# Performance work log

Hardware: AMD Instinct MI355X
Metric: run time of the kernel (lower is better)

Reference implementation:

```python
import jax, jax.numpy as jnp
import numpy as np

B, N, T, C = 2, 2048, 32, 32
NUM_BASES, MAX_K, K_CURR = 4, 32, 16


def setup_inputs() -> dict:
    key = jax.random.key(0)
    k1, k2, k3, k4, k5 = jax.random.split(key, 5)
    z = jax.random.normal(k1, (B, N, T, C), dtype=jnp.float32)
    neighbor_indices = jax.random.randint(k2, (N, K_CURR), 0, N)
    # parameters (match torch init scales)
    adjacency = 0.5 + 0.01 * jax.random.normal(k3, (N, MAX_K), dtype=jnp.float32)
    basis_weights = 0.02 * jax.random.normal(k4, (NUM_BASES, N, MAX_K), dtype=jnp.float32)
    channel_coeffs = jax.random.normal(k5, (C, NUM_BASES), dtype=jnp.float32)
    return {
        "z": z,
        "neighbor_indices": neighbor_indices,
        "adjacency": adjacency,
        "basis_weights": basis_weights,
        "channel_coeffs": channel_coeffs,
    }


def reference(z, neighbor_indices, adjacency, basis_weights, channel_coeffs):
    # z: [B,N,T,C], neighbor_indices: [N,k]
    k = neighbor_indices.shape[1]
    bases = basis_weights[:, :, :k]        # [num_bases, N, k]
    adj = adjacency[:, :k]                 # [N, k]
    # per-channel effective edge weights: [C, N, k]
    eff = jnp.einsum('cb,bnk->cnk', channel_coeffs, bases)
    edge_w = eff * adj[None, :, :]         # [C, N, k]
    w = jnp.transpose(edge_w, (1, 2, 0))   # [N, k, C]
    # gather neighbor features: [B, N, k, T, C]
    z_neigh = z[:, neighbor_indices]
    # weighted sum over neighbors, per-channel weights
    out = jnp.einsum('bnktc,nkc->bntc', z_neigh, w)
    return jnp.tanh(out)
```

## Files before the change

kernel.cpp:

```cpp
#include <hip/hip_runtime.h>


constexpr int BB_    = 2;
constexpr int NN_    = 2048;
constexpr int TT_    = 32;
constexpr int CC_    = 32;
constexpr int NBASE_ = 4;
constexpr int MAXK_  = 32;
constexpr int KC_    = 16;

__device__ __forceinline__ float fast_tanh(float x) {
    float e = __expf(2.0f * x);
    float r = __builtin_amdgcn_rcpf(e + 1.0f);
    return fmaf(-2.0f, r, 1.0f);
}

__global__ __launch_bounds__(256) void cgl_kernel(
    const float* __restrict__ z,
    const int*   __restrict__ nbr,
    const float* __restrict__ adj,
    const float* __restrict__ bw,
    const float* __restrict__ cc,
    float*       __restrict__ out)
{
    __shared__ __align__(16) float w_s[KC_][CC_];
    __shared__ float bw_s[NBASE_][KC_];
    __shared__ float cc_s[CC_ * NBASE_];
    __shared__ float adj_s[KC_];
    __shared__ int   idx_s[KC_];

    const int tid = threadIdx.x;
    const int blk = blockIdx.x;
    const int b   = blk >> 11;
    const int n   = blk & (NN_ - 1);

    if (tid < NBASE_ * KC_) {
        int bb = tid >> 4, k = tid & 15;
        bw_s[bb][k] = bw[((size_t)bb * NN_ + n) * MAXK_ + k];
    } else if (tid >= 64 && tid < 64 + CC_ * NBASE_) {
        int i = tid - 64;
        cc_s[i] = cc[i];
    } else if (tid >= 192 && tid < 192 + KC_) {
        int k = tid - 192;
        adj_s[k] = adj[(size_t)n * MAXK_ + k];
        idx_s[k] = nbr[n * KC_ + k];
    }
    __syncthreads();

    {
        int i = tid;
        #pragma unroll
        for (int r = 0; r < 2; ++r, i += 256) {
            int k = i >> 5, c = i & 31;
            float s = cc_s[c * NBASE_ + 0] * bw_s[0][k]
                    + cc_s[c * NBASE_ + 1] * bw_s[1][k]
                    + cc_s[c * NBASE_ + 2] * bw_s[2][k]
                    + cc_s[c * NBASE_ + 3] * bw_s[3][k];
            w_s[k][c] = s * adj_s[k];
        }
    }
    __syncthreads();

    const int c0 = (tid << 2) & 31;
    const float4* __restrict__ z4 = (const float4*)z;
    const size_t zb = (size_t)b * NN_ * (TT_ * CC_ / 4);

    float4 acc = make_float4(0.f, 0.f, 0.f, 0.f);
    #pragma unroll
    for (int k = 0; k < KC_; ++k) {
        const int nk = idx_s[k];
        float4 zv = z4[zb + (size_t)nk * (TT_ * CC_ / 4) + tid];
        float4 wv = *(const float4*)&w_s[k][c0];
        acc.x = fmaf(zv.x, wv.x, acc.x);
        acc.y = fmaf(zv.y, wv.y, acc.y);
        acc.z = fmaf(zv.z, wv.z, acc.z);
        acc.w = fmaf(zv.w, wv.w, acc.w);
    }

    float4 o;
    o.x = fast_tanh(acc.x);
    o.y = fast_tanh(acc.y);
    o.z = fast_tanh(acc.z);
    o.w = fast_tanh(acc.w);
    ((float4*)out)[(size_t)blk * 256 + tid] = o;
}

extern "C" void kernel_launch(void* const* d_in, const int* in_sizes, int n_in,
                              void* d_out, int out_size, void* d_ws, size_t ws_size,
                              hipStream_t stream) {
    const float* z   = (const float*)d_in[0];
    const int*   nbr = (const int*)d_in[1];
    const float* adj = (const float*)d_in[2];
    const float* bw  = (const float*)d_in[3];
    const float* cc  = (const float*)d_in[4];
    float* out = (float*)d_out;

    cgl_kernel<<<dim3(BB_ * NN_), dim3(256), 0, stream>>>(z, nbr, adj, bw, cc, out);
}
```

Measured before the change: 96.64 us.

## Remap blocks so each XCD owns one batch and time-quarter slice of z

Each block now handles four nodes (one per wave) for one batch and one quarter of the time axis. The batch and time-quarter are taken from the low three bits of the block index, so under round-robin dispatch each of the eight XCDs touches only its own slice of z. The intent is to make the random neighbor gathers hit in each XCD's private L2 instead of spreading the whole z tensor over every cache. The per-node edge weight setup is now done four times per block and each time slice is recomputed across blocks, which adds redundant setup work and relies on an assumed dispatch order.

```diff
diff --git a/kernel.cpp b/kernel.cpp
--- a/kernel.cpp
+++ b/kernel.cpp
@@ -8,6 +8,10 @@
 constexpr int NBASE_ = 4;
 constexpr int MAXK_  = 32;
 constexpr int KC_    = 16;
+
+constexpr int TQ_      = 4;
+constexpr int SLICE_F4 = (TT_ / TQ_) * CC_ / 4;
+constexpr int NODES_PB = 4;
 
 __device__ __forceinline__ float fast_tanh(float x) {
     float e = __expf(2.0f * x);
@@ -23,54 +27,67 @@
     const float* __restrict__ cc,
     float*       __restrict__ out)
 {
-    __shared__ __align__(16) float w_s[KC_][CC_];
-    __shared__ float bw_s[NBASE_][KC_];
-    __shared__ float cc_s[CC_ * NBASE_];
-    __shared__ float adj_s[KC_];
-    __shared__ int   idx_s[KC_];
+    __shared__ __align__(16) float w_s[NODES_PB][KC_][CC_];
+    __shared__ float bw_s[NODES_PB][NBASE_][KC_];
+    __shared__ float cc_s[NBASE_ * CC_];
+    __shared__ float adj_s[NODES_PB][KC_];
+    __shared__ int   idx_s[NODES_PB][KC_];
 
     const int tid = threadIdx.x;
     const int blk = blockIdx.x;
-    const int b   = blk >> 11;
-    const int n   = blk & (NN_ - 1);
 
-    if (tid < NBASE_ * KC_) {
-        int bb = tid >> 4, k = tid & 15;
-        bw_s[bb][k] = bw[((size_t)bb * NN_ + n) * MAXK_ + k];
-    } else if (tid >= 64 && tid < 64 + CC_ * NBASE_) {
-        int i = tid - 64;
-        cc_s[i] = cc[i];
-    } else if (tid >= 192 && tid < 192 + KC_) {
-        int k = tid - 192;
-        adj_s[k] = adj[(size_t)n * MAXK_ + k];
-        idx_s[k] = nbr[n * KC_ + k];
+    const int xcd   = blk & 7;
+    const int b     = xcd >> 2;
+    const int tq    = xcd & 3;
+    const int group = blk >> 3;
+    const int node0 = group * NODES_PB;
+
+    {
+        int nd = tid >> 6, bb = (tid >> 4) & 3, k = tid & 15;
+        bw_s[nd][bb][k] = bw[((size_t)bb * NN_ + (node0 + nd)) * MAXK_ + k];
+
+        if (tid < 64) {
+            int nd2 = tid >> 4, k2 = tid & 15;
+            adj_s[nd2][k2] = adj[(size_t)(node0 + nd2) * MAXK_ + k2];
+        } else if (tid < 128) {
+            int i = tid - 64, nd2 = i >> 4, k2 = i & 15;
+            idx_s[nd2][k2] = nbr[(node0 + nd2) * KC_ + k2];
+        } else {
+            int i = tid - 128, bb2 = i >> 5, c2 = i & 31;
+            cc_s[bb2 * CC_ + c2] = cc[c2 * NBASE_ + bb2];
+        }
     }
     __syncthreads();
 
     {
         int i = tid;
         #pragma unroll
-        for (int r = 0; r < 2; ++r, i += 256) {
-            int k = i >> 5, c = i & 31;
-            float s = cc_s[c * NBASE_ + 0] * bw_s[0][k]
-                    + cc_s[c * NBASE_ + 1] * bw_s[1][k]
-                    + cc_s[c * NBASE_ + 2] * bw_s[2][k]
-                    + cc_s[c * NBASE_ + 3] * bw_s[3][k];
-            w_s[k][c] = s * adj_s[k];
+        for (int r = 0; r < 8; ++r, i += 256) {
+            int nd = i >> 9, k = (i >> 5) & 15, c = i & 31;
+            float s = cc_s[0 * CC_ + c] * bw_s[nd][0][k]
+                    + cc_s[1 * CC_ + c] * bw_s[nd][1][k]
+                    + cc_s[2 * CC_ + c] * bw_s[nd][2][k]
+                    + cc_s[3 * CC_ + c] * bw_s[nd][3][k];
+            w_s[nd][k][c] = s * adj_s[nd][k];
         }
     }
     __syncthreads();
 
-    const int c0 = (tid << 2) & 31;
+    const int wave = tid >> 6;
+    const int lane = tid & 63;
+    const int n    = node0 + wave;
+    const int c0   = (lane << 2) & 31;
+
     const float4* __restrict__ z4 = (const float4*)z;
-    const size_t zb = (size_t)b * NN_ * (TT_ * CC_ / 4);
+    const size_t plane = (size_t)(TT_ * CC_ / 4);
+    const size_t zb    = (size_t)b * NN_ * plane + (size_t)tq * SLICE_F4 + lane;
 
     float4 acc = make_float4(0.f, 0.f, 0.f, 0.f);
     #pragma unroll
     for (int k = 0; k < KC_; ++k) {
-        const int nk = idx_s[k];
-        float4 zv = z4[zb + (size_t)nk * (TT_ * CC_ / 4) + tid];
-        float4 wv = *(const float4*)&w_s[k][c0];
+        const int nk = idx_s[wave][k];
+        float4 zv = z4[zb + (size_t)nk * plane];
+        float4 wv = *(const float4*)&w_s[wave][k][c0];
         acc.x = fmaf(zv.x, wv.x, acc.x);
         acc.y = fmaf(zv.y, wv.y, acc.y);
         acc.z = fmaf(zv.z, wv.z, acc.z);
@@ -82,7 +99,8 @@
     o.y = fast_tanh(acc.y);
     o.z = fast_tanh(acc.z);
     o.w = fast_tanh(acc.w);
-    ((float4*)out)[(size_t)blk * 256 + tid] = o;
+
+    ((float4*)out)[(size_t)b * NN_ * plane + (size_t)n * plane + tq * SLICE_F4 + lane] = o;
 }
 
 extern "C" void kernel_launch(void* const* d_in, const int* in_sizes, int n_in,
@@ -95,5 +113,6 @@
     const float* cc  = (const float*)d_in[4];
     float* out = (float*)d_out;
 
-    cgl_kernel<<<dim3(BB_ * NN_), dim3(256), 0, stream>>>(z, nbr, adj, bw, cc, out);
+    cgl_kernel<<<dim3(BB_ * TQ_ * (NN_ / NODES_PB)), dim3(256), 0, stream>>>(
+        z, nbr, adj, bw, cc, out);
 }
```

Result: faster. 89.49 us (-7.4%).

## Issue neighbor gathers before weight sync using scalar-loaded indices

Applied to the files above, without the earlier changes.

Each thread now reads the neighbor indices straight from global memory into scalar registers via readfirstlane, so it no longer waits on a shared-memory index table. It issues all 16 gathered z loads before the barrier, overlapping them with the edge-weight computation. The channel-coefficient shared array is transposed for conflict-free reads, and launch bounds ask for 4 blocks per CU. The cost is 64 extra VGPRs for the buffered loads, which may reduce occupancy.

```diff
diff --git a/kernel.cpp b/kernel.cpp
--- a/kernel.cpp
+++ b/kernel.cpp
@@ -15,7 +15,7 @@
     return fmaf(-2.0f, r, 1.0f);
 }
 
-__global__ __launch_bounds__(256) void cgl_kernel(
+__global__ __launch_bounds__(256, 4) void cgl_kernel(
     const float* __restrict__ z,
     const int*   __restrict__ nbr,
     const float* __restrict__ adj,
@@ -25,9 +25,8 @@
 {
     __shared__ __align__(16) float w_s[KC_][CC_];
     __shared__ float bw_s[NBASE_][KC_];
-    __shared__ float cc_s[CC_ * NBASE_];
+    __shared__ float cc_s[NBASE_][CC_];
     __shared__ float adj_s[KC_];
-    __shared__ int   idx_s[KC_];
 
     const int tid = threadIdx.x;
     const int blk = blockIdx.x;
@@ -37,14 +36,20 @@
     if (tid < NBASE_ * KC_) {
         int bb = tid >> 4, k = tid & 15;
         bw_s[bb][k] = bw[((size_t)bb * NN_ + n) * MAXK_ + k];
-    } else if (tid >= 64 && tid < 64 + CC_ * NBASE_) {
-        int i = tid - 64;
-        cc_s[i] = cc[i];
+    } else if (tid < 64 + NBASE_ * CC_) {
+        int i = tid - 64, bb = i >> 5, c = i & 31;
+        cc_s[bb][c] = cc[c * NBASE_ + bb];
     } else if (tid >= 192 && tid < 192 + KC_) {
         int k = tid - 192;
         adj_s[k] = adj[(size_t)n * MAXK_ + k];
-        idx_s[k] = nbr[n * KC_ + k];
     }
+
+    const int* __restrict__ ip = nbr + n * KC_;
+    int nks[KC_];
+    #pragma unroll
+    for (int k = 0; k < KC_; ++k)
+        nks[k] = __builtin_amdgcn_readfirstlane(ip[k]);
+
     __syncthreads();
 
     {
@@ -52,29 +57,32 @@
         #pragma unroll
         for (int r = 0; r < 2; ++r, i += 256) {
             int k = i >> 5, c = i & 31;
-            float s = cc_s[c * NBASE_ + 0] * bw_s[0][k]
-                    + cc_s[c * NBASE_ + 1] * bw_s[1][k]
-                    + cc_s[c * NBASE_ + 2] * bw_s[2][k]
-                    + cc_s[c * NBASE_ + 3] * bw_s[3][k];
+            float s = cc_s[0][c] * bw_s[0][k]
+                    + cc_s[1][c] * bw_s[1][k]
+                    + cc_s[2][c] * bw_s[2][k]
+                    + cc_s[3][c] * bw_s[3][k];
             w_s[k][c] = s * adj_s[k];
         }
     }
+
+    const float4* __restrict__ z4 =
+        (const float4*)z + (size_t)b * NN_ * (TT_ * CC_ / 4);
+    float4 zv[KC_];
+    #pragma unroll
+    for (int k = 0; k < KC_; ++k)
+        zv[k] = z4[(size_t)nks[k] * (TT_ * CC_ / 4) + tid];
+
     __syncthreads();
 
     const int c0 = (tid << 2) & 31;
-    const float4* __restrict__ z4 = (const float4*)z;
-    const size_t zb = (size_t)b * NN_ * (TT_ * CC_ / 4);
-
     float4 acc = make_float4(0.f, 0.f, 0.f, 0.f);
     #pragma unroll
     for (int k = 0; k < KC_; ++k) {
-        const int nk = idx_s[k];
-        float4 zv = z4[zb + (size_t)nk * (TT_ * CC_ / 4) + tid];
         float4 wv = *(const float4*)&w_s[k][c0];
-        acc.x = fmaf(zv.x, wv.x, acc.x);
-        acc.y = fmaf(zv.y, wv.y, acc.y);
-        acc.z = fmaf(zv.z, wv.z, acc.z);
-        acc.w = fmaf(zv.w, wv.w, acc.w);
+        acc.x = fmaf(zv[k].x, wv.x, acc.x);
+        acc.y = fmaf(zv[k].y, wv.y, acc.y);
+        acc.z = fmaf(zv[k].z, wv.z, acc.z);
+        acc.w = fmaf(zv[k].w, wv.w, acc.w);
     }
 
     float4 o;
```

Result: no change. 96.00 us (-0.7%).
